# Performance work log

Hardware: AMD Instinct MI355X
Metric: run time of the kernel (lower is better)

## Reference

```python
import jax, jax.numpy as jnp
import numpy as np

LEVELS = ((64, 176), (32, 88), (16, 44), (8, 22))
S_TOTAL = sum(h * w for h, w in LEVELS)  # 14960
C = 128; HH = 8; HD = 16; R = 4; L = 4; P = 8
G = 32; PC_MIN = -4.0; PC_MAX = 4.0
NUM_CLASSES = 17; PROP = 3 + 3 + 4 + 1 + NUM_CLASSES  # 28


def _ln(x, g, b):
    m = x.mean(-1, keepdims=True)
    v = ((x - m) ** 2).mean(-1, keepdims=True)
    return (x - m) * jax.lax.rsqrt(v + 1e-5) * g + b


def setup_inputs() -> dict:
    key = jax.random.key(0)
    ks = jax.random.split(key, 20)
    B, N, CAM = 1, 1024, 6
    d = {}
    d['query'] = jax.random.normal(ks[0], (B, N, C), jnp.float32)
    d['gaussian_props'] = jax.random.normal(ks[1], (B, N, PROP), jnp.float32)
    d['ms_feats'] = jax.random.normal(ks[2], (B, CAM, S_TOTAL, C), jnp.float32)
    d['depth_maps'] = jax.random.uniform(ks[3], (B, CAM, 64, 176), jnp.float32, 0.5, 50.0)
    d['lidar2img'] = jax.random.normal(ks[4], (B, CAM, 4, 4), jnp.float32)
    d['img_h'] = 256
    d['img_w'] = 704
    w = lambda k, shp: jax.random.normal(k, shp, jnp.float32) * 0.02
    d['W_sc'] = w(ks[5], (3, 3, 3, C, C)); d['b_sc'] = jnp.zeros((C,), jnp.float32)
    d['sc_g'] = jnp.ones((C,), jnp.float32); d['sc_b'] = jnp.zeros((C,), jnp.float32)
    d['ref_off_w'] = w(ks[6], (C, R * 3)); d['ref_off_b'] = jnp.zeros((R * 3,), jnp.float32)
    d['off_w'] = w(ks[7], (C, HH * R * L * P * 2)); d['off_b'] = jnp.zeros((HH * R * L * P * 2,), jnp.float32)
    d['aw_w'] = w(ks[8], (C, HH * R * L * P)); d['aw_b'] = jnp.zeros((HH * R * L * P,), jnp.float32)
    d['val_w'] = w(ks[9], (C, C)); d['val_b'] = jnp.zeros((C,), jnp.float32)
    d['out_w'] = w(ks[10], (C, C)); d['out_b'] = jnp.zeros((C,), jnp.float32)
    d['an_g'] = jnp.ones((C,), jnp.float32); d['an_b'] = jnp.zeros((C,), jnp.float32)
    d['f1_w'] = w(ks[11], (C, 4 * C)); d['f1_b'] = jnp.zeros((4 * C,), jnp.float32)
    d['f2_w'] = w(ks[12], (4 * C, C)); d['f2_b'] = jnp.zeros((C,), jnp.float32)
    d['fn_g'] = jnp.ones((C,), jnp.float32); d['fn_b'] = jnp.zeros((C,), jnp.float32)
    d['p1_w'] = w(ks[13], (C, C)); d['p1_b'] = jnp.zeros((C,), jnp.float32)
    d['p2_w'] = w(ks[14], (C, PROP)); d['p2_b'] = jnp.zeros((PROP,), jnp.float32)
    return d


def _forward(query, gaussian_props, ms_feats, depth_maps, lidar2img,
             W_sc, b_sc, sc_g, sc_b, ref_off_w, ref_off_b, off_w, off_b,
             aw_w, aw_b, val_w, val_b, out_w, out_b, an_g, an_b,
             f1_w, f1_b, f2_w, f2_b, fn_g, fn_b, p1_w, p1_b, p2_w, p2_b,
             img_h, img_w):
    B, N, _ = query.shape
    CAM = ms_feats.shape[1]
    means = gaussian_props[..., :3]
    # ---- SparseConv3DBlock: scatter-mean voxelization, 3x3x3 conv, gather back ----
    vs = (PC_MAX - PC_MIN) / G
    vox = jnp.clip(jnp.floor((means - PC_MIN) / vs).astype(jnp.int32), 0, G - 1)
    flat = (vox[..., 0] * G + vox[..., 1]) * G + vox[..., 2]  # [B,N]
    bi = jnp.arange(B)[:, None]
    grid = jnp.zeros((B, G * G * G, C), query.dtype).at[bi, flat].add(query)
    cnt = jnp.zeros((B, G * G * G, 1), query.dtype).at[bi, flat].add(1.0)
    grid = (grid / jnp.maximum(cnt, 1.0)).reshape(B, G, G, G, C)
    grid = jax.lax.conv_general_dilated(grid, W_sc, (1, 1, 1), 'SAME',
                                        dimension_numbers=('NDHWC', 'DHWIO', 'NDHWC')) + b_sc
    grid = jax.nn.gelu(grid).reshape(B, G * G * G, C)
    query = _ln(query + grid[bi, flat], sc_g, sc_b)
    # ---- DeformableAttention3D ----
    fW = jnp.asarray(img_w, query.dtype); fH = jnp.asarray(img_h, query.dtype)
    ref3d = means[:, :, None, :] + (query @ ref_off_w + ref_off_b).reshape(B, N, R, 3)
    pts = jnp.concatenate([ref3d, jnp.ones_like(ref3d[..., :1])], -1)
    proj = jnp.einsum('bcij,bnrj->bcnri', lidar2img, pts)  # [B,CAM,N,R,4]
    z = proj[..., 2]; zc = jnp.maximum(z, 1e-5)
    u = proj[..., 0] / zc; v = proj[..., 1] / zc
    valid = (z > 1e-5) & (u >= 0) & (u < fW) & (v >= 0) & (v < fH)
    Hd, Wd = depth_maps.shape[2], depth_maps.shape[3]
    iu = jnp.clip((u / fW * Wd).astype(jnp.int32), 0, Wd - 1)
    iv = jnp.clip((v / fH * Hd).astype(jnp.int32), 0, Hd - 1)
    ds = jnp.take_along_axis(depth_maps.reshape(B, CAM, Hd * Wd),
                             (iv * Wd + iu).reshape(B, CAM, N * R), axis=2).reshape(B, CAM, N, R)
    wmask = jnp.exp(-jnp.abs(z - ds)) * valid.astype(query.dtype)  # [B,CAM,N,R]
    ref2 = jnp.stack([u / fW, v / fH], -1)  # [B,CAM,N,R,2]
    offs = (query @ off_w + off_b).reshape(B, N, HH, R, L, P, 2)
    attn = jax.nn.softmax((query @ aw_w + aw_b).reshape(B, N, HH, R * L * P), -1)
    attn = attn.reshape(B, N, HH, R, L, P)
    value = (ms_feats @ val_w + val_b).reshape(B, CAM, S_TOTAL, HH, HD)
    out = jnp.zeros((B, N, HH, HD), query.dtype)
    s0 = 0
    for l, (Hl, Wl) in enumerate(LEVELS):
        sz = Hl * Wl
        vl = value[:, :, s0:s0 + sz].transpose(0, 1, 3, 2, 4).reshape(B * CAM, HH, sz, HD)
        s0 += sz
        off_l = offs[:, :, :, :, l]  # [B,N,HH,R,P,2]
        loc = ref2[:, :, :, None, :, None, :] + off_l[:, None] / jnp.array([Wl, Hl], query.dtype)
        # loc: [B,CAM,N,HH,R,P,2] in normalized coords
        x = (loc[..., 0] * Wl - 0.5).transpose(0, 1, 3, 2, 4, 5).reshape(B * CAM, HH, N * R * P)
        y = (loc[..., 1] * Hl - 0.5).transpose(0, 1, 3, 2, 4, 5).reshape(B * CAM, HH, N * R * P)
        x0 = jnp.floor(x); y0 = jnp.floor(y); wx = x - x0; wy = y - y0
        x0i = jnp.clip(x0.astype(jnp.int32), 0, Wl - 1)
        x1i = jnp.clip(x0.astype(jnp.int32) + 1, 0, Wl - 1)
        y0i = jnp.clip(y0.astype(jnp.int32), 0, Hl - 1)
        y1i = jnp.clip(y0.astype(jnp.int32) + 1, 0, Hl - 1)
        g = lambda ix, iy: jnp.take_along_axis(vl, (iy * Wl + ix)[..., None], axis=2)
        samp = (((1 - wx) * (1 - wy))[..., None] * g(x0i, y0i)
                + (wx * (1 - wy))[..., None] * g(x1i, y0i)
                + ((1 - wx) * wy)[..., None] * g(x0i, y1i)
                + (wx * wy)[..., None] * g(x1i, y1i))  # [B*CAM,HH,N*R*P,HD]
        samp = samp.reshape(B, CAM, HH, N, R, P, HD)
        ws = attn[:, :, :, :, l, :][:, None].transpose(0, 1, 3, 2, 4, 5) * wmask[:, :, None, :, :, None]
        out = out + jnp.einsum('bchnrp,bchnrpd->bnhd', ws, samp)
    attn_out = out.reshape(B, N, C) @ out_w + out_b
    query = _ln(query + attn_out, an_g, an_b)
    query = _ln(query + (jax.nn.gelu(query @ f1_w + f1_b) @ f2_w + f2_b), fn_g, fn_b)
    props = gaussian_props + (jax.nn.gelu(query @ p1_w + p1_b) @ p2_w + p2_b)
    return query, props


def reference(query, gaussian_props, ms_feats, depth_maps, lidar2img,
              W_sc, b_sc, sc_g, sc_b, ref_off_w, ref_off_b, off_w, off_b,
              aw_w, aw_b, val_w, val_b, out_w, out_b, an_g, an_b,
              f1_w, f1_b, f2_w, f2_b, fn_g, fn_b, p1_w, p1_b, p2_w, p2_b,
              img_h, img_w):
    return _forward(query, gaussian_props, ms_feats, depth_maps, lidar2img,
                    W_sc, b_sc, sc_g, sc_b, ref_off_w, ref_off_b, off_w, off_b,
                    aw_w, aw_b, val_w, val_b, out_w, out_b, an_g, an_b,
                    f1_w, f1_b, f2_w, f2_b, fn_g, fn_b, p1_w, p1_b, p2_w, p2_b,
                    img_h, img_w)
```

## Files before the change

kernel.cpp:

```cpp
#include <hip/hip_runtime.h>
#include <hip/hip_bf16.h>
#include <math.h>

#define NQ    1024
#define CC    128
#define CAM   6
#define RR    4
#define LL    4
#define PP    8
#define HHD   8
#define HDD   16
#define GG    32
#define S_TOT 14960
#define PROPN 28
#define NTAP  27
#define MVAL  (CAM * S_TOT)
#define NVB   ((MVAL + 63) / 64)
#define ZWT   191

typedef __attribute__((ext_vector_type(8))) short bf16x8;
typedef __attribute__((ext_vector_type(4))) float f32x4;

__device__ __forceinline__ float gelu_tanh(float x) {
    return 0.5f * x * (1.0f + tanhf(0.7978845608028654f * (x + 0.044715f * x * x * x)));
}

__device__ __forceinline__ unsigned short f2bf(float f) {
    union { float f; unsigned int u; } x; x.f = f;
    unsigned int r = (x.u + 0x7FFFu + ((x.u >> 16) & 1u)) >> 16;
    return (unsigned short)r;
}

__device__ __forceinline__ float bf2f(short s) {
    union { unsigned int u; float f; } x;
    x.u = ((unsigned int)(unsigned short)s) << 16;
    return x.f;
}

__global__ __launch_bounds__(256) void k_wt_scatter(
                             const float* __restrict__ Wsc, unsigned short* __restrict__ WscT,
                             const float* __restrict__ valw,
                             const float* __restrict__ outw, unsigned short* __restrict__ outwT,
                             const float* __restrict__ p1w, unsigned short* __restrict__ p1wT,
                             const float* __restrict__ f1w, unsigned short* __restrict__ f1wT,
                             const float* __restrict__ f2w, unsigned short* __restrict__ f2wT,
                             const float* __restrict__ offw, unsigned short* __restrict__ offwT,
                             const float* __restrict__ aww, unsigned short* __restrict__ awwT,
                             const float* __restrict__ p2w, unsigned short* __restrict__ p2wT,
                             const float* __restrict__ p2b, float* __restrict__ p2bp,
                             const float* __restrict__ qin, const float* __restrict__ gp,
                             float* __restrict__ grid, float* __restrict__ cnt,
                             int* __restrict__ flatidx,
                             const float* __restrict__ ms, const float* __restrict__ valb,
                             unsigned short* __restrict__ value) {
    __shared__ union SM {
        float t[64][65];
        struct { bf16x8 Bs[128 * 16]; unsigned short Os[64 * 128]; float sbias[128]; } v;
    } sm;
    __shared__ int sflat[2];
    int z = blockIdx.z;
    int tid = threadIdx.x;

    if (z >= ZWT) {
        int vb = (z - ZWT) * 4 + blockIdx.x * 2 + blockIdx.y;
        if (vb >= NVB) return;
        int m0 = vb * 64;
        int lane = tid & 63, wv = tid >> 6;
        int r = lane & 15, q = lane >> 4;
        unsigned int* Bsw = (unsigned int*)sm.v.Bs;
#pragma unroll
        for (int it = 0; it < 32; ++it) {
            int idx = tid + it * 256;
            int k = (idx >> 7) * 2, nn = idx & 127;
            unsigned int lo = f2bf(valw[k * 128 + nn]);
            unsigned int hi = f2bf(valw[(k + 1) * 128 + nn]);
            Bsw[(nn * 16 + ((k >> 3) ^ (nn & 15))) * 4 + ((k >> 1) & 3)] = lo | (hi << 16);
        }
        if (tid < 128) sm.v.sbias[tid] = valb[tid];
        __syncthreads();

        int row = m0 + wv * 16 + r;
        int mg = min(row, MVAL - 1);
        const float* pA = ms + (size_t)mg * 128;

        f32x4 acc[8];
#pragma unroll
        for (int j = 0; j < 8; ++j)
#pragma unroll
            for (int e = 0; e < 4; ++e) acc[j][e] = 0.f;

#pragma unroll
        for (int ks = 0; ks < 4; ++ks) {
            const float* p = pA + ks * 32 + q * 8;
            float4 a = *(const float4*)p;
            float4 b = *(const float4*)(p + 4);
            bf16x8 af;
            af[0] = (short)f2bf(a.x); af[1] = (short)f2bf(a.y);
            af[2] = (short)f2bf(a.z); af[3] = (short)f2bf(a.w);
            af[4] = (short)f2bf(b.x); af[5] = (short)f2bf(b.y);
            af[6] = (short)f2bf(b.z); af[7] = (short)f2bf(b.w);
            bf16x8 bfr[8];
#pragma unroll
            for (int j = 0; j < 8; ++j)
                bfr[j] = sm.v.Bs[(j * 16 + r) * 16 + ((ks * 4 + q) ^ r)];
#pragma unroll
            for (int j = 0; j < 8; ++j)
                acc[j] = __builtin_amdgcn_mfma_f32_16x16x32_bf16(af, bfr[j], acc[j], 0, 0, 0);
        }

#pragma unroll
        for (int j = 0; j < 8; ++j)
#pragma unroll
            for (int e = 0; e < 4; ++e) {
                int rl = wv * 16 + q * 4 + e;
                sm.v.Os[rl * 128 + j * 16 + r] = f2bf(acc[j][e] + sm.v.sbias[j * 16 + r]);
            }
        __syncthreads();
#pragma unroll
        for (int it = 0; it < 4; ++it) {
            int idx = tid + it * 256;
            int rl = idx >> 4, ch = idx & 15;
            int m = m0 + rl;
            if (m < MVAL)
                *(bf16x8*)(value + (size_t)m * 128 + ch * 8) = *(const bf16x8*)&sm.v.Os[rl * 128 + ch * 8];
        }
        return;
    }

    if (z >= 63) {
        int half = tid >> 7, c = tid & 127;
        int n = ((z - 63) * 4 + (blockIdx.x * 2 + blockIdx.y)) * 2 + half;
        if (c == 0) {
            float mx = gp[n * PROPN + 0], my = gp[n * PROPN + 1], mz = gp[n * PROPN + 2];
            int vx = (int)floorf((mx + 4.0f) * 4.0f);
            int vy = (int)floorf((my + 4.0f) * 4.0f);
            int vz = (int)floorf((mz + 4.0f) * 4.0f);
            vx = min(max(vx, 0), GG - 1);
            vy = min(max(vy, 0), GG - 1);
            vz = min(max(vz, 0), GG - 1);
            int f = (vx * GG + vy) * GG + vz;
            sflat[half] = f;
            flatidx[n] = f;
            atomicAdd(&cnt[f], 1.0f);
        }
        __syncthreads();
        atomicAdd(&grid[(size_t)sflat[half] * CC + c], qin[(size_t)n * CC + c]);
        return;
    }

    int n0 = blockIdx.x * 64, k0 = blockIdx.y * 64;
    if (z == 62) {
#pragma unroll
        for (int it = 0; it < 16; ++it) {
            int idx = tid + it * 256;
            int r = idx >> 6, c = idx & 63;
            sm.t[r][c] = (n0 + c < PROPN) ? p2w[(size_t)(k0 + r) * PROPN + n0 + c] : 0.f;
        }
        __syncthreads();
#pragma unroll
        for (int it = 0; it < 16; ++it) {
            int idx = tid + it * 256;
            int r = idx >> 6, c = idx & 63;
            p2wT[(size_t)(n0 + r) * 128 + k0 + c] = f2bf(sm.t[c][r]);
        }
        if (blockIdx.x == 0 && blockIdx.y == 0 && tid < 128)
            p2bp[tid] = (tid < PROPN) ? p2b[tid] : 0.f;
        return;
    }
    const float* src; unsigned short* dst; int ss, ds;
    if (z < 27)       { src = Wsc + (size_t)z * 16384; dst = WscT + (size_t)z * 16384; ss = 128; ds = 128; }
    else if (z == 27) { src = outw; dst = outwT; ss = 128; ds = 128; }
    else if (z == 28) { src = p1w;  dst = p1wT;  ss = 128; ds = 128; }
    else if (z == 29) { int q = z - 29; src = f1w + q * 128; dst = f1wT + (size_t)q * 16384; ss = 512; ds = 128; }
    else if (z < 33)  { int q = z - 29; src = f1w + q * 128; dst = f1wT + (size_t)q * 16384; ss = 512;  ds = 128; }
    else if (z < 37)  { int q = z - 33; src = f2w + (size_t)q * 16384; dst = f2wT + q * 128; ss = 128;  ds = 512; }
    else if (z < 53)  { int q = z - 37; src = offw + q * 128; dst = offwT + (size_t)q * 16384; ss = 2048; ds = 128; }
    else              { int q = z - 53; src = aww + q * 128;  dst = awwT + (size_t)q * 16384; ss = 1024; ds = 128; }
#pragma unroll
    for (int it = 0; it < 16; ++it) {
        int idx = tid + it * 256;
        int r = idx >> 6, c = idx & 63;
        sm.t[r][c] = src[(size_t)(k0 + r) * ss + n0 + c];
    }
    __syncthreads();
#pragma unroll
    for (int it = 0; it < 16; ++it) {
        int idx = tid + it * 256;
        int r = idx >> 6, c = idx & 63;
        dst[(size_t)(n0 + r) * ds + k0 + c] = f2bf(sm.t[c][r]);
    }
}

__global__ __launch_bounds__(256) void k_conv1m(
    const float* __restrict__ grid, const float* __restrict__ cnt,
    const int* __restrict__ flatidx, const unsigned short* __restrict__ WT,
    float* __restrict__ convacc27) {
    __shared__ bf16x8 As[128 * 16];
    __shared__ bf16x8 Bs[128 * 16];
    __shared__ int   nbase[128];
    __shared__ float nscale[128];
    int tid = threadIdx.x;
    int tap = blockIdx.y;
    int q0 = blockIdx.x * 128;
    int dz = tap / 9 - 1, dy = (tap / 3) % 3 - 1, dx = tap % 3 - 1;

    if (tid < 128) {
        int f = flatidx[q0 + tid];
        int nx = (f >> 10) + dz, ny = ((f >> 5) & 31) + dy, nz = (f & 31) + dx;
        bool ok = (nx >= 0 && nx < GG && ny >= 0 && ny < GG && nz >= 0 && nz < GG);
        int nf = ok ? (nx * GG + ny) * GG + nz : 0;
        nbase[tid] = nf;
        nscale[tid] = ok ? 1.0f / fmaxf(cnt[nf], 1.0f) : 0.f;
    }
    __syncthreads();
#pragma unroll
    for (int it = 0; it < 8; ++it) {
        int idx = tid + it * 256;
        int m = idx >> 4, c = idx & 15;
        const float* p = grid + (size_t)nbase[m] * CC + c * 8;
        float s = nscale[m];
        float4 a = *(const float4*)p;
        float4 b = *(const float4*)(p + 4);
        bf16x8 u;
        u[0] = (short)f2bf(a.x * s); u[1] = (short)f2bf(a.y * s);
        u[2] = (short)f2bf(a.z * s); u[3] = (short)f2bf(a.w * s);
        u[4] = (short)f2bf(b.x * s); u[5] = (short)f2bf(b.y * s);
        u[6] = (short)f2bf(b.z * s); u[7] = (short)f2bf(b.w * s);
        As[m * 16 + (c ^ (m & 15))] = u;
    }
    const unsigned short* Wt = WT + (size_t)tap * CC * CC;
#pragma unroll
    for (int it = 0; it < 8; ++it) {
        int idx = tid + it * 256;
        int n = idx >> 4, c = idx & 15;
        bf16x8 w = *(const bf16x8*)(Wt + (size_t)n * CC + c * 8);
        Bs[n * 16 + (c ^ (n & 15))] = w;
    }
    __syncthreads();

    int lane = tid & 63, wv = tid >> 6;
    int wr = (wv >> 1) * 64, wc = (wv & 1) * 64;
    int r = lane & 15, q = lane >> 4;
    f32x4 acc[4][4];
#pragma unroll
    for (int i = 0; i < 4; ++i)
#pragma unroll
        for (int j = 0; j < 4; ++j)
#pragma unroll
            for (int e = 0; e < 4; ++e) acc[i][j][e] = 0.f;
#pragma unroll
    for (int ks = 0; ks < 4; ++ks) {
        bf16x8 bfr[4];
#pragma unroll
        for (int j = 0; j < 4; ++j)
            bfr[j] = Bs[(wc + j * 16 + r) * 16 + ((ks * 4 + q) ^ r)];
#pragma unroll
        for (int i = 0; i < 4; ++i) {
            bf16x8 af = As[(wr + i * 16 + r) * 16 + ((ks * 4 + q) ^ r)];
#pragma unroll
            for (int j = 0; j < 4; ++j)
                acc[i][j] = __builtin_amdgcn_mfma_f32_16x16x32_bf16(af, bfr[j], acc[i][j], 0, 0, 0);
        }
    }
    float* dst = convacc27 + (size_t)tap * NQ * CC;
#pragma unroll
    for (int i = 0; i < 4; ++i)
#pragma unroll
        for (int e = 0; e < 4; ++e) {
            int m = q0 + wr + i * 16 + q * 4 + e;
#pragma unroll
            for (int j = 0; j < 4; ++j) {
                int col = wc + j * 16 + r;
                dst[(size_t)m * CC + col] = acc[i][j][e];
            }
        }
}

__global__ void k_ln_conv_proj(const float* __restrict__ a, const float* __restrict__ convacc27,
                               const float* __restrict__ bconv,
                               const float* __restrict__ g, const float* __restrict__ be,
                               float* __restrict__ out, unsigned short* __restrict__ outbf,
                               const float* __restrict__ refw, const float* __restrict__ refb,
                               const float* __restrict__ gp, const float* __restrict__ l2i,
                               const float* __restrict__ depth,
                               const int* __restrict__ ih, const int* __restrict__ iw,
                               float* __restrict__ wm, float* __restrict__ r2u,
                               float* __restrict__ r2v) {
    int n = blockIdx.x, c = threadIdx.x;
    float apart = 0.f;
#pragma unroll
    for (int t = 0; t < NTAP; ++t) apart += convacc27[((size_t)t * NQ + n) * CC + c];
    float x = a[n * CC + c] + gelu_tanh(apart + bconv[c]);
    __shared__ float w4[4];
    __shared__ float qrow[CC];
    __shared__ float ro[12];
    float s = x;
#pragma unroll
    for (int d = 1; d < 64; d <<= 1) s += __shfl_xor(s, d);
    if ((c & 63) == 0) w4[c >> 6] = s;
    __syncthreads();
    float m = (w4[0] + w4[1]) * (1.0f / CC);
    float dd = x - m;
    float v = dd * dd;
#pragma unroll
    for (int d = 1; d < 64; d <<= 1) v += __shfl_xor(v, d);
    if ((c & 63) == 0) w4[2 + (c >> 6)] = v;
    __syncthreads();
    float var = (w4[2] + w4[3]) * (1.0f / CC);
    float qv = dd * rsqrtf(var + 1e-5f) * g[c] + be[c];
    out[n * CC + c] = qv;
    outbf[n * CC + c] = f2bf(qv);
    qrow[c] = qv;
    __syncthreads();
    if (c < 12) {
        float sacc = refb[c];
#pragma unroll 4
        for (int k = 0; k < 128; ++k) sacc += qrow[k] * refw[k * 12 + c];
        ro[c] = sacc;
    }
    __syncthreads();
    if (c < 24) {
        int cam = c >> 2, r = c & 3;
        float fH = (float)(*ih), fW = (float)(*iw);
        const float* M = l2i + cam * 16;
        float px = gp[n * PROPN + 0] + ro[r * 3 + 0];
        float py = gp[n * PROPN + 1] + ro[r * 3 + 1];
        float pz = gp[n * PROPN + 2] + ro[r * 3 + 2];
        float p0 = M[0] * px + M[1] * py + M[2]  * pz + M[3];
        float p1 = M[4] * px + M[5] * py + M[6]  * pz + M[7];
        float p2 = M[8] * px + M[9] * py + M[10] * pz + M[11];
        float zc = fmaxf(p2, 1e-5f);
        float u = p0 / zc, vv = p1 / zc;
        bool valid = (p2 > 1e-5f) && (u >= 0.f) && (u < fW) && (vv >= 0.f) && (vv < fH);
        int iu = min(max((int)(u / fW * 176.f), 0), 175);
        int iv = min(max((int)(vv / fH * 64.f), 0), 63);
        float ds = depth[cam * 64 * 176 + iv * 176 + iu];
        int o = cam * (NQ * RR) + n * RR + r;
        wm[o]  = valid ? expf(-fabsf(p2 - ds)) : 0.f;
        r2u[o] = u / fW;
        r2v[o] = vv / fH;
    }
}

__global__ __launch_bounds__(256) void k_qhead(
    const unsigned short* __restrict__ Abf,
    const unsigned short* __restrict__ offwT, const float* __restrict__ offb,
    unsigned short* __restrict__ offsb,
    const unsigned short* __restrict__ awwT, const float* __restrict__ awb,
    unsigned short* __restrict__ attn)
{
    __shared__ bf16x8 Bs[128 * 16];
    bool isoff = blockIdx.x < 16;
    int n0 = (isoff ? blockIdx.x : (blockIdx.x - 16)) * 128;
    const unsigned short* WT = isoff ? offwT : awwT;
    int m0 = blockIdx.y * 128;
    int tid = threadIdx.x, lane = tid & 63, wv = tid >> 6;
    int r = lane & 15, q = lane >> 4;
    int mw = m0 + wv * 32;

#pragma unroll
    for (int it = 0; it < 8; ++it) {
        int idx = tid + it * 256;
        int n = idx >> 4, c = idx & 15;
        Bs[n * 16 + (c ^ (n & 15))] = *(const bf16x8*)(WT + (size_t)(n0 + n) * 128 + c * 8);
    }
    __syncthreads();

    f32x4 acc[2][8];
#pragma unroll
    for (int i = 0; i < 2; ++i)
#pragma unroll
        for (int j = 0; j < 8; ++j)
#pragma unroll
            for (int e = 0; e < 4; ++e) acc[i][j][e] = 0.f;

#pragma unroll
    for (int ks = 0; ks < 4; ++ks) {
        bf16x8 af[2];
#pragma unroll
        for (int i = 0; i < 2; ++i)
            af[i] = *(const bf16x8*)(Abf + (size_t)(mw + i * 16 + r) * 128 + (ks * 4 + q) * 8);
#pragma unroll
        for (int j = 0; j < 8; ++j) {
            bf16x8 b = Bs[(j * 16 + r) * 16 + ((ks * 4 + q) ^ r)];
#pragma unroll
            for (int i = 0; i < 2; ++i)
                acc[i][j] = __builtin_amdgcn_mfma_f32_16x16x32_bf16(af[i], b, acc[i][j], 0, 0, 0);
        }
    }

    float bia[8];
    const float* bsrc = isoff ? offb : awb;
#pragma unroll
    for (int j = 0; j < 8; ++j) bia[j] = bsrc[n0 + j * 16 + r];

    if (isoff) {
#pragma unroll
        for (int i = 0; i < 2; ++i)
#pragma unroll
            for (int e = 0; e < 4; ++e) {
                int m = mw + i * 16 + q * 4 + e;
                unsigned short* orow = offsb + (size_t)m * 2048 + n0;
#pragma unroll
                for (int j = 0; j < 8; ++j)
                    orow[j * 16 + r] = f2bf(acc[i][j][e] + bia[j]);
            }
    } else {
#pragma unroll
        for (int i = 0; i < 2; ++i)
#pragma unroll
            for (int e = 0; e < 4; ++e) {
                float mx = -1e30f;
#pragma unroll
                for (int j = 0; j < 8; ++j) mx = fmaxf(mx, acc[i][j][e] + bia[j]);
#pragma unroll
                for (int d = 1; d < 16; d <<= 1) mx = fmaxf(mx, __shfl_xor(mx, d));
                float ex[8];
                float sum = 0.f;
#pragma unroll
                for (int j = 0; j < 8; ++j) { ex[j] = expf(acc[i][j][e] + bia[j] - mx); sum += ex[j]; }
#pragma unroll
                for (int d = 1; d < 16; d <<= 1) sum += __shfl_xor(sum, d);
                float inv = 1.0f / sum;
                int m = mw + i * 16 + q * 4 + e;
                unsigned short* orow = attn + (size_t)m * 1024 + n0;
#pragma unroll
                for (int j = 0; j < 8; ++j)
                    orow[j * 16 + r] = f2bf(ex[j] * inv);
            }
    }
}

__global__ __launch_bounds__(512) void k_sample(
                         const unsigned short* __restrict__ value,
                         const unsigned short* __restrict__ offsb,
                         const unsigned short* __restrict__ attn,
                         const float* __restrict__ wm,
                         const float* __restrict__ r2u, const float* __restrict__ r2v,
                         float* __restrict__ sampout) {
    const int Wl_[4] = {176, 88, 44, 22};
    const int Hl_[4] = {64, 32, 16, 8};
    const int s0_[4] = {0, 11264, 14080, 14784};
    int n = blockIdx.x, tid = threadIdx.x;
    __shared__ float s_attn[1024];
    __shared__ float s_offs[2048];
    __shared__ float s_wm[24], s_ru[24], s_rv[24];
    __shared__ float part[HHD][HDD];

    if (tid < 128) {
        bf16x8 v = *(const bf16x8*)(attn + (size_t)n * 1024 + tid * 8);
#pragma unroll
        for (int d = 0; d < 8; ++d) s_attn[tid * 8 + d] = bf2f(v[d]);
    }
    if (tid < 256) {
        bf16x8 v = *(const bf16x8*)(offsb + (size_t)n * 2048 + tid * 8);
#pragma unroll
        for (int d = 0; d < 8; ++d) s_offs[tid * 8 + d] = bf2f(v[d]);
    }
    if (tid < 24) {
        int cam = tid >> 2, r = tid & 3;
        int o = cam * (NQ * RR) + n * RR + r;
        s_wm[tid] = wm[o]; s_ru[tid] = r2u[o]; s_rv[tid] = r2v[o];
    }
    __syncthreads();

    int half = tid >> 8;
    int t8 = tid & 255;
    int h = t8 >> 5, slot = t8 & 31;
    int l = slot >> 3, p = slot & 7;
    int Wl = Wl_[l], Hl = Hl_[l];
    float fWl = (float)Wl, fHl = (float)Hl;
    float acc[16];
#pragma unroll
    for (int d = 0; d < 16; ++d) acc[d] = 0.f;

    for (int cr = half * 12; cr < half * 12 + 12; ++cr) {
        int cam = cr >> 2, r = cr & 3;
        float ws = s_attn[h * 128 + r * 32 + l * 8 + p] * s_wm[cr];
        if (ws == 0.f) continue;
        float ox = s_offs[h * 256 + r * 64 + l * 16 + p * 2 + 0];
        float oy = s_offs[h * 256 + r * 64 + l * 16 + p * 2 + 1];
        float x = s_ru[cr] * fWl + ox - 0.5f;
        float y = s_rv[cr] * fHl + oy - 0.5f;
        float xf = floorf(x), yf = floorf(y);
        float wx = x - xf, wy = y - yf;
        int x0 = min(max((int)xf, 0), Wl - 1);
        int x1 = min(max((int)xf + 1, 0), Wl - 1);
        int y0 = min(max((int)yf, 0), Hl - 1);
        int y1 = min(max((int)yf + 1, 0), Hl - 1);
        size_t b = ((size_t)cam * S_TOT + s0_[l]) * CC + h * HDD;
        const unsigned short* p00 = value + b + (size_t)(y0 * Wl + x0) * CC;
        const unsigned short* p01 = value + b + (size_t)(y0 * Wl + x1) * CC;
        const unsigned short* p10 = value + b + (size_t)(y1 * Wl + x0) * CC;
        const unsigned short* p11 = value + b + (size_t)(y1 * Wl + x1) * CC;
        float w00 = ws * (1.f - wx) * (1.f - wy);
        float w01 = ws * wx * (1.f - wy);
        float w10 = ws * (1.f - wx) * wy;
        float w11 = ws * wx * wy;
        bf16x8 va0 = *(const bf16x8*)p00, va1 = *(const bf16x8*)(p00 + 8);
        bf16x8 vb0 = *(const bf16x8*)p01, vb1 = *(const bf16x8*)(p01 + 8);
        bf16x8 vc0 = *(const bf16x8*)p10, vc1 = *(const bf16x8*)(p10 + 8);
        bf16x8 vd0 = *(const bf16x8*)p11, vd1 = *(const bf16x8*)(p11 + 8);
#pragma unroll
        for (int d = 0; d < 8; ++d)
            acc[d] += w00 * bf2f(va0[d]) + w01 * bf2f(vb0[d]) + w10 * bf2f(vc0[d]) + w11 * bf2f(vd0[d]);
#pragma unroll
        for (int d = 0; d < 8; ++d)
            acc[8 + d] += w00 * bf2f(va1[d]) + w01 * bf2f(vb1[d]) + w10 * bf2f(vc1[d]) + w11 * bf2f(vd1[d]);
    }

#pragma unroll
    for (int d = 0; d < 16; ++d) {
        float a = acc[d];
#pragma unroll
        for (int s = 16; s >= 1; s >>= 1) a += __shfl_xor(a, s, 32);
        acc[d] = a;
    }
    if (half == 1 && slot == 0) {
#pragma unroll
        for (int d = 0; d < 16; ++d) part[h][d] = acc[d];
    }
    __syncthreads();
    if (half == 0 && slot == 0) {
#pragma unroll
        for (int d = 0; d < 16; ++d)
            sampout[(size_t)n * CC + h * HDD + d] = acc[d] + part[h][d];
    }
}

__global__ __launch_bounds__(256) void k_tail(
    const float* __restrict__ sampout,
    const unsigned short* __restrict__ outwT, const float* __restrict__ outb,
    const float* __restrict__ q1, const float* __restrict__ ang, const float* __restrict__ anb,
    const unsigned short* __restrict__ f1wT, const float* __restrict__ f1b,
    const unsigned short* __restrict__ f2wT, const float* __restrict__ f2b,
    const float* __restrict__ fng, const float* __restrict__ fnb,
    const unsigned short* __restrict__ p1wT, const float* __restrict__ p1b,
    const unsigned short* __restrict__ p2wT, const float* __restrict__ p2bp,
    const float* __restrict__ gp, float* __restrict__ outq, float* __restrict__ outp)
{
    __shared__ bf16x8 As[16 * 16];
    __shared__ bf16x8 Aff[16 * 64];
    __shared__ float xrow[16 * 128];
    __shared__ float q2s[16 * 128];
    unsigned short* Affu = (unsigned short*)Aff;
    unsigned short* As2u = (unsigned short*)Aff;
    int tid = threadIdx.x, m0 = blockIdx.x * 16;
    int lane = tid & 63, wv = tid >> 6;
    int wc = wv * 32;
    int r = lane & 15, q = lane >> 4;
    int lrow = tid >> 4, ls = tid & 15;

    bf16x8 b1[2][4];
#pragma unroll
    for (int j = 0; j < 2; ++j)
#pragma unroll
        for (int ks = 0; ks < 4; ++ks)
            b1[j][ks] = *(const bf16x8*)(outwT + (size_t)(wc + j * 16 + r) * 128 + (ks * 4 + q) * 8);

    {
        int m = tid >> 4, c = tid & 15;
        const float* p = sampout + (size_t)(m0 + m) * 128 + c * 8;
        float4 a = *(const float4*)p;
        float4 b = *(const float4*)(p + 4);
        bf16x8 u;
        u[0] = (short)f2bf(a.x); u[1] = (short)f2bf(a.y);
        u[2] = (short)f2bf(a.z); u[3] = (short)f2bf(a.w);
        u[4] = (short)f2bf(b.x); u[5] = (short)f2bf(b.y);
        u[6] = (short)f2bf(b.z); u[7] = (short)f2bf(b.w);
        As[m * 16 + (c ^ m)] = u;
    }
    __syncthreads();

    f32x4 acc[2];
    bf16x8 a4[4];
#pragma unroll
    for (int ks = 0; ks < 4; ++ks) a4[ks] = As[r * 16 + ((ks * 4 + q) ^ r)];
#pragma unroll
    for (int j = 0; j < 2; ++j)
#pragma unroll
        for (int e = 0; e < 4; ++e) acc[j][e] = 0.f;
#pragma unroll
    for (int ks = 0; ks < 4; ++ks)
#pragma unroll
        for (int j = 0; j < 2; ++j)
            acc[j] = __builtin_amdgcn_mfma_f32_16x16x32_bf16(a4[ks], b1[j][ks], acc[j], 0, 0, 0);
#pragma unroll
    for (int e = 0; e < 4; ++e) {
        int ml = q * 4 + e;
#pragma unroll
        for (int j = 0; j < 2; ++j) {
            int cl = wc + j * 16 + r;
            xrow[ml * 128 + cl] = acc[j][e] + outb[cl] + q1[(size_t)(m0 + ml) * 128 + cl];
        }
    }
    __syncthreads();

    {
        float* xr = xrow + lrow * 128;
        float sum = 0.f;
#pragma unroll
        for (int e = ls; e < 128; e += 16) sum += xr[e];
#pragma unroll
        for (int d = 8; d; d >>= 1) sum += __shfl_xor(sum, d, 16);
        float mean = sum * (1.0f / 128.0f);
        float var = 0.f;
#pragma unroll
        for (int e = ls; e < 128; e += 16) { float dd = xr[e] - mean; var += dd * dd; }
#pragma unroll
        for (int d = 8; d; d >>= 1) var += __shfl_xor(var, d, 16);
        float rstd = rsqrtf(var * (1.0f / 128.0f) + 1e-5f);
#pragma unroll
        for (int e = ls; e < 128; e += 16)
            q2s[lrow * 128 + e] = (xr[e] - mean) * rstd * ang[e] + anb[e];
    }
    __syncthreads();
    {
        int m = tid >> 4, c = tid & 15;
        const float* p = q2s + m * 128 + c * 8;
        bf16x8 u;
#pragma unroll
        for (int d = 0; d < 8; ++d) u[d] = (short)f2bf(p[d]);
        As[m * 16 + (c ^ m)] = u;
    }
    __syncthreads();

#pragma unroll
    for (int ks = 0; ks < 4; ++ks) a4[ks] = As[r * 16 + ((ks * 4 + q) ^ r)];
    bf16x8 bcur[2][4];
#pragma unroll
    for (int j = 0; j < 2; ++j)
#pragma unroll
        for (int ks = 0; ks < 4; ++ks)
            bcur[j][ks] = *(const bf16x8*)(f1wT + (size_t)(wc + j * 16 + r) * 128 + (ks * 4 + q) * 8);
#pragma unroll
    for (int nt = 0; nt < 4; ++nt) {
        bf16x8 bnx[2][4];
        if (nt < 3) {
#pragma unroll
            for (int j = 0; j < 2; ++j)
#pragma unroll
                for (int ks = 0; ks < 4; ++ks)
                    bnx[j][ks] = *(const bf16x8*)(f1wT + (size_t)(nt + 1) * 16384
                                                  + (size_t)(wc + j * 16 + r) * 128 + (ks * 4 + q) * 8);
        }
#pragma unroll
        for (int j = 0; j < 2; ++j)
#pragma unroll
            for (int e = 0; e < 4; ++e) acc[j][e] = 0.f;
#pragma unroll
        for (int ks = 0; ks < 4; ++ks)
#pragma unroll
            for (int j = 0; j < 2; ++j)
                acc[j] = __builtin_amdgcn_mfma_f32_16x16x32_bf16(a4[ks], bcur[j][ks], acc[j], 0, 0, 0);
#pragma unroll
        for (int e = 0; e < 4; ++e) {
            int ml = q * 4 + e;
#pragma unroll
            for (int j = 0; j < 2; ++j) {
                int col = nt * 128 + wc + j * 16 + r;
                float v = gelu_tanh(acc[j][e] + f1b[col]);
                Affu[(ml * 64 + ((col >> 3) ^ ml)) * 8 + (col & 7)] = f2bf(v);
            }
        }
        if (nt < 3) {
#pragma unroll
            for (int j = 0; j < 2; ++j)
#pragma unroll
                for (int ks = 0; ks < 4; ++ks) bcur[j][ks] = bnx[j][ks];
        }
    }
    __syncthreads();

#pragma unroll
    for (int j = 0; j < 2; ++j)
#pragma unroll
        for (int e = 0; e < 4; ++e) acc[j][e] = 0.f;
#pragma unroll
    for (int j = 0; j < 2; ++j)
#pragma unroll
        for (int ks = 0; ks < 4; ++ks)
            bcur[j][ks] = *(const bf16x8*)(f2wT + (size_t)(wc + j * 16 + r) * 512 + (ks * 4 + q) * 8);
#pragma unroll
    for (int kc = 0; kc < 4; ++kc) {
        bf16x8 bnx[2][4];
        if (kc < 3) {
#pragma unroll
            for (int j = 0; j < 2; ++j)
#pragma unroll
                for (int ks = 0; ks < 4; ++ks)
                    bnx[j][ks] = *(const bf16x8*)(f2wT + (size_t)(wc + j * 16 + r) * 512
                                                  + ((kc + 1) * 16 + ks * 4 + q) * 8);
        }
#pragma unroll
        for (int ks = 0; ks < 4; ++ks) {
            bf16x8 af = Aff[r * 64 + ((kc * 16 + ks * 4 + q) ^ r)];
#pragma unroll
            for (int j = 0; j < 2; ++j)
                acc[j] = __builtin_amdgcn_mfma_f32_16x16x32_bf16(af, bcur[j][ks], acc[j], 0, 0, 0);
        }
        if (kc < 3) {
#pragma unroll
            for (int j = 0; j < 2; ++j)
#pragma unroll
                for (int ks = 0; ks < 4; ++ks) bcur[j][ks] = bnx[j][ks];
        }
    }
#pragma unroll
    for (int e = 0; e < 4; ++e) {
        int ml = q * 4 + e;
#pragma unroll
        for (int j = 0; j < 2; ++j) {
            int cl = wc + j * 16 + r;
            xrow[ml * 128 + cl] = acc[j][e] + f2b[cl] + q2s[ml * 128 + cl];
        }
    }
    __syncthreads();

    {
        float* xr = xrow + lrow * 128;
        float sum = 0.f;
#pragma unroll
        for (int e = ls; e < 128; e += 16) sum += xr[e];
#pragma unroll
        for (int d = 8; d; d >>= 1) sum += __shfl_xor(sum, d, 16);
        float mean = sum * (1.0f / 128.0f);
        float var = 0.f;
#pragma unroll
        for (int e = ls; e < 128; e += 16) { float dd = xr[e] - mean; var += dd * dd; }
#pragma unroll
        for (int d = 8; d; d >>= 1) var += __shfl_xor(var, d, 16);
        float rstd = rsqrtf(var * (1.0f / 128.0f) + 1e-5f);
        float* oq = outq + (size_t)(m0 + lrow) * 128;
#pragma unroll
        for (int e = ls; e < 128; e += 16) {
            float v = (xr[e] - mean) * rstd * fng[e] + fnb[e];
            oq[e] = v;
            q2s[lrow * 128 + e] = v;
        }
    }
    __syncthreads();
    {
        int m = tid >> 4, c = tid & 15;
        const float* p = q2s + m * 128 + c * 8;
        bf16x8 u;
#pragma unroll
        for (int d = 0; d < 8; ++d) u[d] = (short)f2bf(p[d]);
        As[m * 16 + (c ^ m)] = u;
    }
    __syncthreads();

#pragma unroll
    for (int ks = 0; ks < 4; ++ks) a4[ks] = As[r * 16 + ((ks * 4 + q) ^ r)];
#pragma unroll
    for (int j = 0; j < 2; ++j) {
#pragma unroll
        for (int ks = 0; ks < 4; ++ks)
            bcur[j][ks] = *(const bf16x8*)(p1wT + (size_t)(wc + j * 16 + r) * 128 + (ks * 4 + q) * 8);
#pragma unroll
        for (int e = 0; e < 4; ++e) acc[j][e] = 0.f;
    }
#pragma unroll
    for (int j = 0; j < 2; ++j)
#pragma unroll
        for (int ks = 0; ks < 4; ++ks)
            b1[j][ks] = *(const bf16x8*)(p2wT + (size_t)(wc + j * 16 + r) * 128 + (ks * 4 + q) * 8);
#pragma unroll
    for (int ks = 0; ks < 4; ++ks)
#pragma unroll
        for (int j = 0; j < 2; ++j)
            acc[j] = __builtin_amdgcn_mfma_f32_16x16x32_bf16(a4[ks], bcur[j][ks], acc[j], 0, 0, 0);
#pragma unroll
    for (int e = 0; e < 4; ++e) {
        int ml = q * 4 + e;
#pragma unroll
        for (int j = 0; j < 2; ++j) {
            int cl = wc + j * 16 + r;
            float v = gelu_tanh(acc[j][e] + p1b[cl]);
            As2u[(ml * 16 + ((cl >> 3) ^ ml)) * 8 + (cl & 7)] = f2bf(v);
        }
    }
    __syncthreads();

#pragma unroll
    for (int j = 0; j < 2; ++j)
#pragma unroll
        for (int e = 0; e < 4; ++e) acc[j][e] = 0.f;
#pragma unroll
    for (int ks = 0; ks < 4; ++ks) {
        bf16x8 af = Aff[r * 16 + ((ks * 4 + q) ^ r)];
#pragma unroll
        for (int j = 0; j < 2; ++j)
            acc[j] = __builtin_amdgcn_mfma_f32_16x16x32_bf16(af, b1[j][ks], acc[j], 0, 0, 0);
    }
#pragma unroll
    for (int e = 0; e < 4; ++e) {
        int m = m0 + q * 4 + e;
#pragma unroll
        for (int j = 0; j < 2; ++j) {
            int cl = wc + j * 16 + r;
            if (cl < PROPN)
                outp[(size_t)m * PROPN + cl] = acc[j][e] + p2bp[cl] + gp[(size_t)m * PROPN + cl];
        }
    }
}

extern "C" void kernel_launch(void* const* d_in, const int* in_sizes, int n_in,
                              void* d_out, int out_size, void* d_ws, size_t ws_size,
                              hipStream_t stream) {
    const float* query = (const float*)d_in[0];
    const float* gp    = (const float*)d_in[1];
    const float* ms    = (const float*)d_in[2];
    const float* depth = (const float*)d_in[3];
    const float* l2i   = (const float*)d_in[4];
    const int*   ih    = (const int*)d_in[5];
    const int*   iw    = (const int*)d_in[6];
    const float* Wsc   = (const float*)d_in[7];
    const float* bsc   = (const float*)d_in[8];
    const float* scg   = (const float*)d_in[9];
    const float* scb   = (const float*)d_in[10];
    const float* refw  = (const float*)d_in[11];
    const float* refb  = (const float*)d_in[12];
    const float* offw  = (const float*)d_in[13];
    const float* offbi = (const float*)d_in[14];
    const float* aww   = (const float*)d_in[15];
    const float* awb   = (const float*)d_in[16];
    const float* valw  = (const float*)d_in[17];
    const float* valb  = (const float*)d_in[18];
    const float* outw  = (const float*)d_in[19];
    const float* outb  = (const float*)d_in[20];
    const float* ang   = (const float*)d_in[21];
    const float* anb   = (const float*)d_in[22];
    const float* f1w   = (const float*)d_in[23];
    const float* f1b   = (const float*)d_in[24];
    const float* f2w   = (const float*)d_in[25];
    const float* f2b   = (const float*)d_in[26];
    const float* fng   = (const float*)d_in[27];
    const float* fnb   = (const float*)d_in[28];
    const float* p1w   = (const float*)d_in[29];
    const float* p1b   = (const float*)d_in[30];
    const float* p2w   = (const float*)d_in[31];
    const float* p2b   = (const float*)d_in[32];

    float* outq = (float*)d_out;
    float* outp = outq + NQ * CC;

    float* ws = (float*)d_ws;
    size_t o = 0;
    float* grid    = ws + o; o += (size_t)GG * GG * GG * CC;
    float* cnt     = ws + o; o += GG * GG * GG;
    size_t zero_floats = o;
    int*   flatidx = (int*)(ws + o); o += NQ;
    float* convacc27 = ws + o; o += (size_t)NTAP * NQ * CC;
    float* q1      = ws + o; o += NQ * CC;
    float* wm      = ws + o; o += CAM * NQ * RR;
    float* r2u     = ws + o; o += CAM * NQ * RR;
    float* r2v     = ws + o; o += CAM * NQ * RR;
    float* sampout = ws + o; o += NQ * CC;
    float* p2bp    = ws + o; o += 128;
    unsigned short* u16base = (unsigned short*)(ws + o);
    size_t uo = 0;
    unsigned short* value = u16base + uo; uo += (size_t)CAM * S_TOT * CC;
    unsigned short* offsb = u16base + uo; uo += (size_t)NQ * 2048;
    unsigned short* attn  = u16base + uo; uo += (size_t)NQ * 1024;
    unsigned short* q1bf  = u16base + uo; uo += (size_t)NQ * CC;
    unsigned short* offwT = u16base + uo; uo += (size_t)2048 * 128;
    unsigned short* awwT  = u16base + uo; uo += (size_t)1024 * 128;
    unsigned short* outwT = u16base + uo; uo += 128 * 128;
    unsigned short* f1wT  = u16base + uo; uo += 512 * 128;
    unsigned short* f2wT  = u16base + uo; uo += 128 * 512;
    unsigned short* p1wT  = u16base + uo; uo += 128 * 128;
    unsigned short* p2wT  = u16base + uo; uo += 128 * 128;
    unsigned short* WscT  = u16base + uo; uo += (size_t)27 * 128 * 128;
    (void)ws_size; (void)in_sizes; (void)n_in; (void)out_size;

    hipMemsetAsync(ws, 0, zero_floats * sizeof(float), stream);

    int zvp = (NVB + 3) / 4;
    k_wt_scatter<<<dim3(2, 2, ZWT + zvp), 256, 0, stream>>>(
        Wsc, WscT, valw, outw, outwT, p1w, p1wT, f1w, f1wT, f2w, f2wT,
        offw, offwT, aww, awwT, p2w, p2wT, p2b, p2bp,
        query, gp, grid, cnt, flatidx,
        ms, valb, value);

    k_conv1m<<<dim3(8, 27), 256, 0, stream>>>(grid, cnt, flatidx, WscT, convacc27);
    k_ln_conv_proj<<<NQ, CC, 0, stream>>>(query, convacc27, bsc, scg, scb, q1, q1bf,
                                          refw, refb, gp, l2i, depth, ih, iw, wm, r2u, r2v);

    k_qhead<<<dim3(24, 8), 256, 0, stream>>>(q1bf, offwT, offbi, offsb, awwT, awb, attn);
    k_sample<<<NQ, 512, 0, stream>>>(value, offsb, attn, wm, r2u, r2v, sampout);

    k_tail<<<64, 256, 0, stream>>>(sampout, outwT, outb, q1, ang, anb,
                                   f1wT, f1b, f2wT, f2b, fng, fnb,
                                   p1wT, p1b, p2wT, p2bp, gp, outq, outp);
}
```

Before: 225.4 us.

## Move value projection into qhead kernel, use head-planar value layout, widen tail

The value projection GEMM moves out of the weight-transpose/scatter kernel and into the query-head kernel, which now reads a pre-transposed bf16 value weight. The value tensor is stored head-planar per level (position-major within each head) so that the sampling kernel's bilinear taps read contiguous 16-element head slices. The tail kernel now runs with 512 threads, each wave computing one 16-column tile, and layernorm is spread over 32 lanes. This trades the earlier overlap of the value GEMM with the weight prep for better gather locality and more parallelism in the tail.

```diff
diff --git a/kernel.cpp b/kernel.cpp
--- a/kernel.cpp
+++ b/kernel.cpp
@@ -16,7 +16,6 @@
 #define NTAP  27
 #define MVAL  (CAM * S_TOT)
 #define NVB   ((MVAL + 63) / 64)
-#define ZWT   191
 
 typedef __attribute__((ext_vector_type(8))) short bf16x8;
 typedef __attribute__((ext_vector_type(4))) float f32x4;
@@ -37,9 +36,8 @@
     return x.f;
 }
 
-__global__ __launch_bounds__(256) void k_wt_scatter(
-                             const float* __restrict__ Wsc, unsigned short* __restrict__ WscT,
-                             const float* __restrict__ valw,
+__global__ void k_wt_scatter(const float* __restrict__ Wsc, unsigned short* __restrict__ WscT,
+                             const float* __restrict__ valw, unsigned short* __restrict__ valwT,
                              const float* __restrict__ outw, unsigned short* __restrict__ outwT,
                              const float* __restrict__ p1w, unsigned short* __restrict__ p1wT,
                              const float* __restrict__ f1w, unsigned short* __restrict__ f1wT,
@@ -50,82 +48,11 @@
                              const float* __restrict__ p2b, float* __restrict__ p2bp,
                              const float* __restrict__ qin, const float* __restrict__ gp,
                              float* __restrict__ grid, float* __restrict__ cnt,
-                             int* __restrict__ flatidx,
-                             const float* __restrict__ ms, const float* __restrict__ valb,
-                             unsigned short* __restrict__ value) {
-    __shared__ union SM {
-        float t[64][65];
-        struct { bf16x8 Bs[128 * 16]; unsigned short Os[64 * 128]; float sbias[128]; } v;
-    } sm;
+                             int* __restrict__ flatidx) {
+    __shared__ float t[64][65];
     __shared__ int sflat[2];
     int z = blockIdx.z;
     int tid = threadIdx.x;
-
-    if (z >= ZWT) {
-        int vb = (z - ZWT) * 4 + blockIdx.x * 2 + blockIdx.y;
-        if (vb >= NVB) return;
-        int m0 = vb * 64;
-        int lane = tid & 63, wv = tid >> 6;
-        int r = lane & 15, q = lane >> 4;
-        unsigned int* Bsw = (unsigned int*)sm.v.Bs;
-#pragma unroll
-        for (int it = 0; it < 32; ++it) {
-            int idx = tid + it * 256;
-            int k = (idx >> 7) * 2, nn = idx & 127;
-            unsigned int lo = f2bf(valw[k * 128 + nn]);
-            unsigned int hi = f2bf(valw[(k + 1) * 128 + nn]);
-            Bsw[(nn * 16 + ((k >> 3) ^ (nn & 15))) * 4 + ((k >> 1) & 3)] = lo | (hi << 16);
-        }
-        if (tid < 128) sm.v.sbias[tid] = valb[tid];
-        __syncthreads();
-
-        int row = m0 + wv * 16 + r;
-        int mg = min(row, MVAL - 1);
-        const float* pA = ms + (size_t)mg * 128;
-
-        f32x4 acc[8];
-#pragma unroll
-        for (int j = 0; j < 8; ++j)
-#pragma unroll
-            for (int e = 0; e < 4; ++e) acc[j][e] = 0.f;
-
-#pragma unroll
-        for (int ks = 0; ks < 4; ++ks) {
-            const float* p = pA + ks * 32 + q * 8;
-            float4 a = *(const float4*)p;
-            float4 b = *(const float4*)(p + 4);
-            bf16x8 af;
-            af[0] = (short)f2bf(a.x); af[1] = (short)f2bf(a.y);
-            af[2] = (short)f2bf(a.z); af[3] = (short)f2bf(a.w);
-            af[4] = (short)f2bf(b.x); af[5] = (short)f2bf(b.y);
-            af[6] = (short)f2bf(b.z); af[7] = (short)f2bf(b.w);
-            bf16x8 bfr[8];
-#pragma unroll
-            for (int j = 0; j < 8; ++j)
-                bfr[j] = sm.v.Bs[(j * 16 + r) * 16 + ((ks * 4 + q) ^ r)];
-#pragma unroll
-            for (int j = 0; j < 8; ++j)
-                acc[j] = __builtin_amdgcn_mfma_f32_16x16x32_bf16(af, bfr[j], acc[j], 0, 0, 0);
-        }
-
-#pragma unroll
-        for (int j = 0; j < 8; ++j)
-#pragma unroll
-            for (int e = 0; e < 4; ++e) {
-                int rl = wv * 16 + q * 4 + e;
-                sm.v.Os[rl * 128 + j * 16 + r] = f2bf(acc[j][e] + sm.v.sbias[j * 16 + r]);
-            }
-        __syncthreads();
-#pragma unroll
-        for (int it = 0; it < 4; ++it) {
-            int idx = tid + it * 256;
-            int rl = idx >> 4, ch = idx & 15;
-            int m = m0 + rl;
-            if (m < MVAL)
-                *(bf16x8*)(value + (size_t)m * 128 + ch * 8) = *(const bf16x8*)&sm.v.Os[rl * 128 + ch * 8];
-        }
-        return;
-    }
 
     if (z >= 63) {
         int half = tid >> 7, c = tid & 127;
@@ -154,14 +81,14 @@
         for (int it = 0; it < 16; ++it) {
             int idx = tid + it * 256;
             int r = idx >> 6, c = idx & 63;
-            sm.t[r][c] = (n0 + c < PROPN) ? p2w[(size_t)(k0 + r) * PROPN + n0 + c] : 0.f;
+            t[r][c] = (n0 + c < PROPN) ? p2w[(size_t)(k0 + r) * PROPN + n0 + c] : 0.f;
         }
         __syncthreads();
 #pragma unroll
         for (int it = 0; it < 16; ++it) {
             int idx = tid + it * 256;
             int r = idx >> 6, c = idx & 63;
-            p2wT[(size_t)(n0 + r) * 128 + k0 + c] = f2bf(sm.t[c][r]);
+            p2wT[(size_t)(n0 + r) * 128 + k0 + c] = f2bf(t[c][r]);
         }
         if (blockIdx.x == 0 && blockIdx.y == 0 && tid < 128)
             p2bp[tid] = (tid < PROPN) ? p2b[tid] : 0.f;
@@ -169,25 +96,25 @@
     }
     const float* src; unsigned short* dst; int ss, ds;
     if (z < 27)       { src = Wsc + (size_t)z * 16384; dst = WscT + (size_t)z * 16384; ss = 128; ds = 128; }
-    else if (z == 27) { src = outw; dst = outwT; ss = 128; ds = 128; }
-    else if (z == 28) { src = p1w;  dst = p1wT;  ss = 128; ds = 128; }
-    else if (z == 29) { int q = z - 29; src = f1w + q * 128; dst = f1wT + (size_t)q * 16384; ss = 512; ds = 128; }
-    else if (z < 33)  { int q = z - 29; src = f1w + q * 128; dst = f1wT + (size_t)q * 16384; ss = 512;  ds = 128; }
-    else if (z < 37)  { int q = z - 33; src = f2w + (size_t)q * 16384; dst = f2wT + q * 128; ss = 128;  ds = 512; }
-    else if (z < 53)  { int q = z - 37; src = offw + q * 128; dst = offwT + (size_t)q * 16384; ss = 2048; ds = 128; }
-    else              { int q = z - 53; src = aww + q * 128;  dst = awwT + (size_t)q * 16384; ss = 1024; ds = 128; }
+    else if (z == 27) { src = valw; dst = valwT; ss = 128; ds = 128; }
+    else if (z == 28) { src = outw; dst = outwT; ss = 128; ds = 128; }
+    else if (z == 29) { src = p1w;  dst = p1wT;  ss = 128; ds = 128; }
+    else if (z < 34)  { int q = z - 30; src = f1w + q * 128; dst = f1wT + (size_t)q * 16384; ss = 512;  ds = 128; }
+    else if (z < 38)  { int q = z - 34; src = f2w + (size_t)q * 16384; dst = f2wT + q * 128; ss = 128;  ds = 512; }
+    else if (z < 54)  { int q = z - 38; src = offw + q * 128; dst = offwT + (size_t)q * 16384; ss = 2048; ds = 128; }
+    else              { int q = z - 54; src = aww + q * 128;  dst = awwT + (size_t)q * 16384; ss = 1024; ds = 128; }
 #pragma unroll
     for (int it = 0; it < 16; ++it) {
         int idx = tid + it * 256;
         int r = idx >> 6, c = idx & 63;
-        sm.t[r][c] = src[(size_t)(k0 + r) * ss + n0 + c];
+        t[r][c] = src[(size_t)(k0 + r) * ss + n0 + c];
     }
     __syncthreads();
 #pragma unroll
     for (int it = 0; it < 16; ++it) {
         int idx = tid + it * 256;
         int r = idx >> 6, c = idx & 63;
-        dst[(size_t)(n0 + r) * ds + k0 + c] = f2bf(sm.t[c][r]);
+        dst[(size_t)(n0 + r) * ds + k0 + c] = f2bf(t[c][r]);
     }
 }
 
@@ -342,27 +269,107 @@
     }
 }
 
-__global__ __launch_bounds__(256) void k_qhead(
+union QVSm {
+    bf16x8 Bs[128 * 16];
+    struct { bf16x8 Bs[128 * 16]; unsigned short Os[64 * 128]; float sbias[128]; } v;
+};
+__global__ __launch_bounds__(256) void k_qhead_val(
     const unsigned short* __restrict__ Abf,
     const unsigned short* __restrict__ offwT, const float* __restrict__ offb,
     unsigned short* __restrict__ offsb,
     const unsigned short* __restrict__ awwT, const float* __restrict__ awb,
-    unsigned short* __restrict__ attn)
+    unsigned short* __restrict__ attn,
+    const float* __restrict__ ms, const unsigned short* __restrict__ valwT,
+    const float* __restrict__ valb, unsigned short* __restrict__ value)
 {
-    __shared__ bf16x8 Bs[128 * 16];
-    bool isoff = blockIdx.x < 16;
-    int n0 = (isoff ? blockIdx.x : (blockIdx.x - 16)) * 128;
+    __shared__ QVSm sm;
+    int bx = blockIdx.x, tid = threadIdx.x;
+    int lane = tid & 63, wv = tid >> 6;
+    int r = lane & 15, q = lane >> 4;
+
+    if (bx >= 24) {
+        int vb = (bx - 24) * 8 + blockIdx.y;
+        if (vb >= NVB) return;
+        int m0 = vb * 64;
+#pragma unroll
+        for (int it = 0; it < 8; ++it) {
+            int idx = tid + it * 256;
+            int n = idx >> 4, c = idx & 15;
+            sm.v.Bs[n * 16 + (c ^ (n & 15))] = *(const bf16x8*)(valwT + (size_t)n * 128 + c * 8);
+        }
+        if (tid < 128) sm.v.sbias[tid] = valb[tid];
+        __syncthreads();
+
+        int row = m0 + wv * 16 + r;
+        int mg = min(row, MVAL - 1);
+        const float* pA = ms + (size_t)mg * 128;
+
+        f32x4 acc[8];
+#pragma unroll
+        for (int j = 0; j < 8; ++j)
+#pragma unroll
+            for (int e = 0; e < 4; ++e) acc[j][e] = 0.f;
+
+#pragma unroll
+        for (int ks = 0; ks < 4; ++ks) {
+            const float* p = pA + ks * 32 + q * 8;
+            float4 a = *(const float4*)p;
+            float4 b = *(const float4*)(p + 4);
+            bf16x8 af;
+            af[0] = (short)f2bf(a.x); af[1] = (short)f2bf(a.y);
+            af[2] = (short)f2bf(a.z); af[3] = (short)f2bf(a.w);
+            af[4] = (short)f2bf(b.x); af[5] = (short)f2bf(b.y);
+            af[6] = (short)f2bf(b.z); af[7] = (short)f2bf(b.w);
+            bf16x8 bfr[8];
+#pragma unroll
+            for (int j = 0; j < 8; ++j)
+                bfr[j] = sm.v.Bs[(j * 16 + r) * 16 + ((ks * 4 + q) ^ r)];
+#pragma unroll
+            for (int j = 0; j < 8; ++j)
+                acc[j] = __builtin_amdgcn_mfma_f32_16x16x32_bf16(af, bfr[j], acc[j], 0, 0, 0);
+        }
+
+#pragma unroll
+        for (int j = 0; j < 8; ++j)
+#pragma unroll
+            for (int e = 0; e < 4; ++e) {
+                int rl = wv * 16 + q * 4 + e;
+                sm.v.Os[rl * 128 + j * 16 + r] = f2bf(acc[j][e] + sm.v.sbias[j * 16 + r]);
+            }
+        __syncthreads();
+#pragma unroll
+        for (int it = 0; it < 2; ++it) {
+            int idx = tid + it * 256;
+            int rl = idx & 63, h = idx >> 6;
+            int m = m0 + rl;
+            if (m < MVAL) {
+                int cam = m / S_TOT;
+                int s = m - cam * S_TOT;
+                int pos, HW, sb;
+                if (s < 11264)      { pos = s;          HW = 11264; sb = 0; }
+                else if (s < 14080) { pos = s - 11264;  HW = 2816;  sb = 11264; }
+                else if (s < 14784) { pos = s - 14080;  HW = 704;   sb = 14080; }
+                else                { pos = s - 14784;  HW = 176;   sb = 14784; }
+                size_t dst = ((size_t)cam * S_TOT + sb) * CC
+                           + (size_t)h * (HW * HDD) + (size_t)pos * HDD;
+                *(bf16x8*)(value + dst)     = *(const bf16x8*)&sm.v.Os[rl * 128 + h * 16];
+                *(bf16x8*)(value + dst + 8) = *(const bf16x8*)&sm.v.Os[rl * 128 + h * 16 + 8];
+            }
+        }
+        return;
+    }
+
+    bool isoff = bx < 16;
+    int n0 = (isoff ? bx : (bx - 16)) * 128;
     const unsigned short* WT = isoff ? offwT : awwT;
     int m0 = blockIdx.y * 128;
-    int tid = threadIdx.x, lane = tid & 63, wv = tid >> 6;
-    int r = lane & 15, q = lane >> 4;
     int mw = m0 + wv * 32;
 
 #pragma unroll
     for (int it = 0; it < 8; ++it) {
         int idx = tid + it * 256;
         int n = idx >> 4, c = idx & 15;
-        Bs[n * 16 + (c ^ (n & 15))] = *(const bf16x8*)(WT + (size_t)(n0 + n) * 128 + c * 8);
+        sm.Bs[n * 16 + (c ^ (n & 15))] = *(const bf16x8*)(WT + (size_t)(n0 + n) * 128 + c * 8);
     }
     __syncthreads();
 
@@ -382,7 +389,7 @@
             af[i] = *(const bf16x8*)(Abf + (size_t)(mw + i * 16 + r) * 128 + (ks * 4 + q) * 8);
 #pragma unroll
         for (int j = 0; j < 8; ++j) {
-            bf16x8 b = Bs[(j * 16 + r) * 16 + ((ks * 4 + q) ^ r)];
+            bf16x8 b = sm.Bs[(j * 16 + r) * 16 + ((ks * 4 + q) ^ r)];
 #pragma unroll
             for (int i = 0; i < 2; ++i)
                 acc[i][j] = __builtin_amdgcn_mfma_f32_16x16x32_bf16(af[i], b, acc[i][j], 0, 0, 0);
@@ -470,6 +477,7 @@
     int l = slot >> 3, p = slot & 7;
     int Wl = Wl_[l], Hl = Hl_[l];
     float fWl = (float)Wl, fHl = (float)Hl;
+    size_t planeC = (size_t)s0_[l] * CC + (size_t)h * (Hl * Wl * HDD);
     float acc[16];
 #pragma unroll
     for (int d = 0; d < 16; ++d) acc[d] = 0.f;
@@ -488,11 +496,11 @@
         int x1 = min(max((int)xf + 1, 0), Wl - 1);
         int y0 = min(max((int)yf, 0), Hl - 1);
         int y1 = min(max((int)yf + 1, 0), Hl - 1);
-        size_t b = ((size_t)cam * S_TOT + s0_[l]) * CC + h * HDD;
-        const unsigned short* p00 = value + b + (size_t)(y0 * Wl + x0) * CC;
-        const unsigned short* p01 = value + b + (size_t)(y0 * Wl + x1) * CC;
-        const unsigned short* p10 = value + b + (size_t)(y1 * Wl + x0) * CC;
-        const unsigned short* p11 = value + b + (size_t)(y1 * Wl + x1) * CC;
+        const unsigned short* base = value + (size_t)cam * S_TOT * CC + planeC;
+        const unsigned short* p00 = base + (size_t)(y0 * Wl + x0) * HDD;
+        const unsigned short* p01 = base + (size_t)(y0 * Wl + x1) * HDD;
+        const unsigned short* p10 = base + (size_t)(y1 * Wl + x0) * HDD;
+        const unsigned short* p11 = base + (size_t)(y1 * Wl + x1) * HDD;
         float w00 = ws * (1.f - wx) * (1.f - wy);
         float w01 = ws * wx * (1.f - wy);
         float w10 = ws * (1.f - wx) * wy;
@@ -528,7 +536,7 @@
     }
 }
 
-__global__ __launch_bounds__(256) void k_tail(
+__global__ __launch_bounds__(512) void k_tail(
     const float* __restrict__ sampout,
     const unsigned short* __restrict__ outwT, const float* __restrict__ outb,
     const float* __restrict__ q1, const float* __restrict__ ang, const float* __restrict__ anb,
@@ -547,18 +555,16 @@
     unsigned short* As2u = (unsigned short*)Aff;
     int tid = threadIdx.x, m0 = blockIdx.x * 16;
     int lane = tid & 63, wv = tid >> 6;
-    int wc = wv * 32;
+    int wc = wv * 16;
     int r = lane & 15, q = lane >> 4;
-    int lrow = tid >> 4, ls = tid & 15;
-
-    bf16x8 b1[2][4];
-#pragma unroll
-    for (int j = 0; j < 2; ++j)
-#pragma unroll
-        for (int ks = 0; ks < 4; ++ks)
-            b1[j][ks] = *(const bf16x8*)(outwT + (size_t)(wc + j * 16 + r) * 128 + (ks * 4 + q) * 8);
-
-    {
+    int lrow = tid >> 5, ls = tid & 31;
+
+    bf16x8 b1[4];
+#pragma unroll
+    for (int ks = 0; ks < 4; ++ks)
+        b1[ks] = *(const bf16x8*)(outwT + (size_t)(wc + r) * 128 + (ks * 4 + q) * 8);
+
+    if (tid < 256) {
         int m = tid >> 4, c = tid & 15;
         const float* p = sampout + (size_t)(m0 + m) * 128 + c * 8;
         float4 a = *(const float4*)p;
@@ -572,27 +578,20 @@
     }
     __syncthreads();
 
-    f32x4 acc[2];
+    f32x4 acc;
     bf16x8 a4[4];
 #pragma unroll
     for (int ks = 0; ks < 4; ++ks) a4[ks] = As[r * 16 + ((ks * 4 + q) ^ r)];
 #pragma unroll
-    for (int j = 0; j < 2; ++j)
-#pragma unroll
-        for (int e = 0; e < 4; ++e) acc[j][e] = 0.f;
+    for (int e = 0; e < 4; ++e) acc[e] = 0.f;
 #pragma unroll
     for (int ks = 0; ks < 4; ++ks)
-#pragma unroll
-        for (int j = 0; j < 2; ++j)
-            acc[j] = __builtin_amdgcn_mfma_f32_16x16x32_bf16(a4[ks], b1[j][ks], acc[j], 0, 0, 0);
+        acc = __builtin_amdgcn_mfma_f32_16x16x32_bf16(a4[ks], b1[ks], acc, 0, 0, 0);
 #pragma unroll
     for (int e = 0; e < 4; ++e) {
         int ml = q * 4 + e;
-#pragma unroll
-        for (int j = 0; j < 2; ++j) {
-            int cl = wc + j * 16 + r;
-            xrow[ml * 128 + cl] = acc[j][e] + outb[cl] + q1[(size_t)(m0 + ml) * 128 + cl];
-        }
+        int cl = wc + r;
+        xrow[ml * 128 + cl] = acc[e] + outb[cl] + q1[(size_t)(m0 + ml) * 128 + cl];
     }
     __syncthreads();
 
@@ -600,22 +599,22 @@
         float* xr = xrow + lrow * 128;
         float sum = 0.f;
 #pragma unroll
-        for (int e = ls; e < 128; e += 16) sum += xr[e];
-#pragma unroll
-        for (int d = 8; d; d >>= 1) sum += __shfl_xor(sum, d, 16);
+        for (int e = ls; e < 128; e += 32) sum += xr[e];
+#pragma unroll
+        for (int d = 16; d; d >>= 1) sum += __shfl_xor(sum, d, 32);
         float mean = sum * (1.0f / 128.0f);
         float var = 0.f;
 #pragma unroll
-        for (int e = ls; e < 128; e += 16) { float dd = xr[e] - mean; var += dd * dd; }
-#pragma unroll
-        for (int d = 8; d; d >>= 1) var += __shfl_xor(var, d, 16);
+        for (int e = ls; e < 128; e += 32) { float dd = xr[e] - mean; var += dd * dd; }
+#pragma unroll
+        for (int d = 16; d; d >>= 1) var += __shfl_xor(var, d, 32);
         float rstd = rsqrtf(var * (1.0f / 128.0f) + 1e-5f);
 #pragma unroll
-        for (int e = ls; e < 128; e += 16)
+        for (int e = ls; e < 128; e += 32)
             q2s[lrow * 128 + e] = (xr[e] - mean) * rstd * ang[e] + anb[e];
     }
     __syncthreads();
-    {
+    if (tid < 256) {
         int m = tid >> 4, c = tid & 15;
         const float* p = q2s + m * 128 + c * 8;
         bf16x8 u;
@@ -627,93 +626,67 @@
 
 #pragma unroll
     for (int ks = 0; ks < 4; ++ks) a4[ks] = As[r * 16 + ((ks * 4 + q) ^ r)];
-    bf16x8 bcur[2][4];
-#pragma unroll
-    for (int j = 0; j < 2; ++j)
+    bf16x8 bcur[4];
+#pragma unroll
+    for (int ks = 0; ks < 4; ++ks)
+        bcur[ks] = *(const bf16x8*)(f1wT + (size_t)(wc + r) * 128 + (ks * 4 + q) * 8);
+#pragma unroll
+    for (int nt = 0; nt < 4; ++nt) {
+        bf16x8 bnx[4];
+        if (nt < 3) {
+#pragma unroll
+            for (int ks = 0; ks < 4; ++ks)
+                bnx[ks] = *(const bf16x8*)(f1wT + (size_t)(nt + 1) * 16384
+                                            + (size_t)(wc + r) * 128 + (ks * 4 + q) * 8);
+        }
+#pragma unroll
+        for (int e = 0; e < 4; ++e) acc[e] = 0.f;
 #pragma unroll
         for (int ks = 0; ks < 4; ++ks)
-            bcur[j][ks] = *(const bf16x8*)(f1wT + (size_t)(wc + j * 16 + r) * 128 + (ks * 4 + q) * 8);
-#pragma unroll
-    for (int nt = 0; nt < 4; ++nt) {
-        bf16x8 bnx[2][4];
-        if (nt < 3) {
-#pragma unroll
-            for (int j = 0; j < 2; ++j)
-#pragma unroll
-                for (int ks = 0; ks < 4; ++ks)
-                    bnx[j][ks] = *(const bf16x8*)(f1wT + (size_t)(nt + 1) * 16384
-                                                  + (size_t)(wc + j * 16 + r) * 128 + (ks * 4 + q) * 8);
-        }
-#pragma unroll
-        for (int j = 0; j < 2; ++j)
-#pragma unroll
-            for (int e = 0; e < 4; ++e) acc[j][e] = 0.f;
-#pragma unroll
-        for (int ks = 0; ks < 4; ++ks)
-#pragma unroll
-            for (int j = 0; j < 2; ++j)
-                acc[j] = __builtin_amdgcn_mfma_f32_16x16x32_bf16(a4[ks], bcur[j][ks], acc[j], 0, 0, 0);
+            acc = __builtin_amdgcn_mfma_f32_16x16x32_bf16(a4[ks], bcur[ks], acc, 0, 0, 0);
 #pragma unroll
         for (int e = 0; e < 4; ++e) {
             int ml = q * 4 + e;
-#pragma unroll
-            for (int j = 0; j < 2; ++j) {
-                int col = nt * 128 + wc + j * 16 + r;
-                float v = gelu_tanh(acc[j][e] + f1b[col]);
-                Affu[(ml * 64 + ((col >> 3) ^ ml)) * 8 + (col & 7)] = f2bf(v);
-            }
+            int col = nt * 128 + wc + r;
+            float v = gelu_tanh(acc[e] + f1b[col]);
+            Affu[(ml * 64 + ((col >> 3) ^ ml)) * 8 + (col & 7)] = f2bf(v);
         }
         if (nt < 3) {
 #pragma unroll
-            for (int j = 0; j < 2; ++j)
-#pragma unroll
-                for (int ks = 0; ks < 4; ++ks) bcur[j][ks] = bnx[j][ks];
-        }
-    }
-    __syncthreads();
-
-#pragma unroll
-    for (int j = 0; j < 2; ++j)
-#pragma unroll
-        for (int e = 0; e < 4; ++e) acc[j][e] = 0.f;
-#pragma unroll
-    for (int j = 0; j < 2; ++j)
-#pragma unroll
-        for (int ks = 0; ks < 4; ++ks)
-            bcur[j][ks] = *(const bf16x8*)(f2wT + (size_t)(wc + j * 16 + r) * 512 + (ks * 4 + q) * 8);
+            for (int ks = 0; ks < 4; ++ks) bcur[ks] = bnx[ks];
+        }
+    }
+    __syncthreads();
+
+#pragma unroll
+    for (int e = 0; e < 4; ++e) acc[e] = 0.f;
+#pragma unroll
+    for (int ks = 0; ks < 4; ++ks)
+        bcur[ks] = *(const bf16x8*)(f2wT + (size_t)(wc + r) * 512 + (ks * 4 + q) * 8);
 #pragma unroll
     for (int kc = 0; kc < 4; ++kc) {
-        bf16x8 bnx[2][4];
+        bf16x8 bnx[4];
         if (kc < 3) {
 #pragma unroll
-            for (int j = 0; j < 2; ++j)
-#pragma unroll
-                for (int ks = 0; ks < 4; ++ks)
-                    bnx[j][ks] = *(const bf16x8*)(f2wT + (size_t)(wc + j * 16 + r) * 512
-                                                  + ((kc + 1) * 16 + ks * 4 + q) * 8);
+            for (int ks = 0; ks < 4; ++ks)
+                bnx[ks] = *(const bf16x8*)(f2wT + (size_t)(wc + r) * 512
+                                            + ((kc + 1) * 16 + ks * 4 + q) * 8);
         }
 #pragma unroll
         for (int ks = 0; ks < 4; ++ks) {
             bf16x8 af = Aff[r * 64 + ((kc * 16 + ks * 4 + q) ^ r)];
-#pragma unroll
-            for (int j = 0; j < 2; ++j)
-                acc[j] = __builtin_amdgcn_mfma_f32_16x16x32_bf16(af, bcur[j][ks], acc[j], 0, 0, 0);
+            acc = __builtin_amdgcn_mfma_f32_16x16x32_bf16(af, bcur[ks], acc, 0, 0, 0);
         }
         if (kc < 3) {
 #pragma unroll
-            for (int j = 0; j < 2; ++j)
-#pragma unroll
-                for (int ks = 0; ks < 4; ++ks) bcur[j][ks] = bnx[j][ks];
+            for (int ks = 0; ks < 4; ++ks) bcur[ks] = bnx[ks];
         }
     }
 #pragma unroll
     for (int e = 0; e < 4; ++e) {
         int ml = q * 4 + e;
-#pragma unroll
-        for (int j = 0; j < 2; ++j) {
-            int cl = wc + j * 16 + r;
-            xrow[ml * 128 + cl] = acc[j][e] + f2b[cl] + q2s[ml * 128 + cl];
-        }
+        int cl = wc + r;
+        xrow[ml * 128 + cl] = acc[e] + f2b[cl] + q2s[ml * 128 + cl];
     }
     __syncthreads();
 
@@ -721,26 +694,26 @@
         float* xr = xrow + lrow * 128;
         float sum = 0.f;
 #pragma unroll
-        for (int e = ls; e < 128; e += 16) sum += xr[e];
-#pragma unroll
-        for (int d = 8; d; d >>= 1) sum += __shfl_xor(sum, d, 16);
+        for (int e = ls; e < 128; e += 32) sum += xr[e];
+#pragma unroll
+        for (int d = 16; d; d >>= 1) sum += __shfl_xor(sum, d, 32);
         float mean = sum * (1.0f / 128.0f);
         float var = 0.f;
 #pragma unroll
-        for (int e = ls; e < 128; e += 16) { float dd = xr[e] - mean; var += dd * dd; }
-#pragma unroll
-        for (int d = 8; d; d >>= 1) var += __shfl_xor(var, d, 16);
+        for (int e = ls; e < 128; e += 32) { float dd = xr[e] - mean; var += dd * dd; }
+#pragma unroll
+        for (int d = 16; d; d >>= 1) var += __shfl_xor(var, d, 32);
         float rstd = rsqrtf(var * (1.0f / 128.0f) + 1e-5f);
         float* oq = outq + (size_t)(m0 + lrow) * 128;
 #pragma unroll
-        for (int e = ls; e < 128; e += 16) {
+        for (int e = ls; e < 128; e += 32) {
             float v = (xr[e] - mean) * rstd * fng[e] + fnb[e];
             oq[e] = v;
             q2s[lrow * 128 + e] = v;
         }
     }
     __syncthreads();
-    {
+    if (tid < 256) {
         int m = tid >> 4, c = tid & 15;
         const float* p = q2s + m * 128 + c * 8;
         bf16x8 u;
@@ -753,55 +726,38 @@
 #pragma unroll
     for (int ks = 0; ks < 4; ++ks) a4[ks] = As[r * 16 + ((ks * 4 + q) ^ r)];
 #pragma unroll
-    for (int j = 0; j < 2; ++j) {
-#pragma unroll
-        for (int ks = 0; ks < 4; ++ks)
-            bcur[j][ks] = *(const bf16x8*)(p1wT + (size_t)(wc + j * 16 + r) * 128 + (ks * 4 + q) * 8);
-#pragma unroll
-        for (int e = 0; e < 4; ++e) acc[j][e] = 0.f;
-    }
-#pragma unroll
-    for (int j = 0; j < 2; ++j)
-#pragma unroll
-        for (int ks = 0; ks < 4; ++ks)
-            b1[j][ks] = *(const bf16x8*)(p2wT + (size_t)(wc + j * 16 + r) * 128 + (ks * 4 + q) * 8);
-#pragma unroll
     for (int ks = 0; ks < 4; ++ks)
-#pragma unroll
-        for (int j = 0; j < 2; ++j)
-            acc[j] = __builtin_amdgcn_mfma_f32_16x16x32_bf16(a4[ks], bcur[j][ks], acc[j], 0, 0, 0);
+        bcur[ks] = *(const bf16x8*)(p1wT + (size_t)(wc + r) * 128 + (ks * 4 + q) * 8);
+#pragma unroll
+    for (int ks = 0; ks < 4; ++ks)
+        b1[ks] = *(const bf16x8*)(p2wT + (size_t)(wc + r) * 128 + (ks * 4 + q) * 8);
+#pragma unroll
+    for (int e = 0; e < 4; ++e) acc[e] = 0.f;
+#pragma unroll
+    for (int ks = 0; ks < 4; ++ks)
+        acc = __builtin_amdgcn_mfma_f32_16x16x32_bf16(a4[ks], bcur[ks], acc, 0, 0, 0);
 #pragma unroll
     for (int e = 0; e < 4; ++e) {
         int ml = q * 4 + e;
-#pragma unroll
-        for (int j = 0; j < 2; ++j) {
-            int cl = wc + j * 16 + r;
-            float v = gelu_tanh(acc[j][e] + p1b[cl]);
-            As2u[(ml * 16 + ((cl >> 3) ^ ml)) * 8 + (cl & 7)] = f2bf(v);
-        }
-    }
-    __syncthreads();
-
-#pragma unroll
-    for (int j = 0; j < 2; ++j)
-#pragma unroll
-        for (int e = 0; e < 4; ++e) acc[j][e] = 0.f;
+        int cl = wc + r;
+        float v = gelu_tanh(acc[e] + p1b[cl]);
+        As2u[(ml * 16 + ((cl >> 3) ^ ml)) * 8 + (cl & 7)] = f2bf(v);
+    }
+    __syncthreads();
+
+#pragma unroll
+    for (int e = 0; e < 4; ++e) acc[e] = 0.f;
 #pragma unroll
     for (int ks = 0; ks < 4; ++ks) {
         bf16x8 af = Aff[r * 16 + ((ks * 4 + q) ^ r)];
-#pragma unroll
-        for (int j = 0; j < 2; ++j)
-            acc[j] = __builtin_amdgcn_mfma_f32_16x16x32_bf16(af, b1[j][ks], acc[j], 0, 0, 0);
+        acc = __builtin_amdgcn_mfma_f32_16x16x32_bf16(af, b1[ks], acc, 0, 0, 0);
     }
 #pragma unroll
     for (int e = 0; e < 4; ++e) {
         int m = m0 + q * 4 + e;
-#pragma unroll
-        for (int j = 0; j < 2; ++j) {
-            int cl = wc + j * 16 + r;
-            if (cl < PROPN)
-                outp[(size_t)m * PROPN + cl] = acc[j][e] + p2bp[cl] + gp[(size_t)m * PROPN + cl];
-        }
+        int cl = wc + r;
+        if (cl < PROPN)
+            outp[(size_t)m * PROPN + cl] = acc[e] + p2bp[cl] + gp[(size_t)m * PROPN + cl];
     }
 }
 
@@ -866,6 +822,7 @@
     unsigned short* q1bf  = u16base + uo; uo += (size_t)NQ * CC;
     unsigned short* offwT = u16base + uo; uo += (size_t)2048 * 128;
     unsigned short* awwT  = u16base + uo; uo += (size_t)1024 * 128;
+    unsigned short* valwT = u16base + uo; uo += 128 * 128;
     unsigned short* outwT = u16base + uo; uo += 128 * 128;
     unsigned short* f1wT  = u16base + uo; uo += 512 * 128;
     unsigned short* f2wT  = u16base + uo; uo += 128 * 512;
@@ -876,21 +833,22 @@
 
     hipMemsetAsync(ws, 0, zero_floats * sizeof(float), stream);
 
-    int zvp = (NVB + 3) / 4;
-    k_wt_scatter<<<dim3(2, 2, ZWT + zvp), 256, 0, stream>>>(
-        Wsc, WscT, valw, outw, outwT, p1w, p1wT, f1w, f1wT, f2w, f2wT,
+    k_wt_scatter<<<dim3(2, 2, 63 + 128), 256, 0, stream>>>(
+        Wsc, WscT, valw, valwT, outw, outwT, p1w, p1wT, f1w, f1wT, f2w, f2wT,
         offw, offwT, aww, awwT, p2w, p2wT, p2b, p2bp,
-        query, gp, grid, cnt, flatidx,
-        ms, valb, value);
+        query, gp, grid, cnt, flatidx);
 
     k_conv1m<<<dim3(8, 27), 256, 0, stream>>>(grid, cnt, flatidx, WscT, convacc27);
     k_ln_conv_proj<<<NQ, CC, 0, stream>>>(query, convacc27, bsc, scg, scb, q1, q1bf,
                                           refw, refb, gp, l2i, depth, ih, iw, wm, r2u, r2v);
 
-    k_qhead<<<dim3(24, 8), 256, 0, stream>>>(q1bf, offwT, offbi, offsb, awwT, awb, attn);
+    k_qhead_val<<<dim3(24 + 176, 8), 256, 0, stream>>>(
+        q1bf, offwT, offbi, offsb, awwT, awb, attn,
+        ms, valwT, valb, value);
+
     k_sample<<<NQ, 512, 0, stream>>>(value, offsb, attn, wm, r2u, r2v, sampout);
 
-    k_tail<<<64, 256, 0, stream>>>(sampout, outwT, outb, q1, ang, anb,
+    k_tail<<<64, 512, 0, stream>>>(sampout, outwT, outb, q1, ang, anb,
                                    f1wT, f1b, f2wT, f2b, fng, fnb,
                                    p1wT, p1b, p2wT, p2bp, gp, outq, outp);
 }
```

Result: no change. 221.5 us (-1.8%).
